# Optimization experiments

Measured on AMD Instinct MI355X. Metric: run time of the kernel, lower is better.

## Reference

```python
import jax, jax.numpy as jnp
import numpy as np

B, T, D, H = 256, 512, 128, 256


def setup_inputs() -> dict:
    key = jax.random.key(0)
    ks = jax.random.split(key, 8)
    return {
        "x": jax.random.normal(ks[0], (B, T, D), jnp.float32),
        "m": jax.random.randint(ks[1], (B, T, D), 0, 2, jnp.int32),
        "s": jax.random.uniform(ks[2], (B, T, 1), jnp.float32),
        "kernel": jax.random.normal(ks[3], (D, 3 * H), jnp.float32) * 0.05,
        "recurrent_kernel": jax.random.normal(ks[4], (H, 3 * H), jnp.float32) * 0.05,
        "masking_kernel": jax.random.normal(ks[5], (D, 3 * H), jnp.float32) * 0.05,
        "bias": jnp.zeros((3 * H,), jnp.float32),
        "input_decay_kernel": jax.random.normal(ks[6], (D,), jnp.float32) * 0.05,
        "input_decay_bias": jnp.zeros((D,), jnp.float32),
        "hidden_decay_kernel": jax.random.normal(ks[7], (D, H), jnp.float32) * 0.05,
        "hidden_decay_bias": jnp.zeros((H,), jnp.float32),
    }


def _grud_scan(x, m, s, kernel, recurrent_kernel, masking_kernel, bias,
               input_decay_kernel, input_decay_bias,
               hidden_decay_kernel, hidden_decay_bias):
    b, t, d = x.shape
    h = recurrent_kernel.shape[0]
    mf = m.astype(x.dtype)
    mb = m > 0  # boolean mask, K.switch semantics
    # mask projection is h-independent -> hoist the big GEMM out of the scan
    mproj = jnp.einsum('btd,dk->btk', mf, masking_kernel)  # [B,T,3H]
    Kz, Kr, Kh = kernel[:, :h], kernel[:, h:2 * h], kernel[:, 2 * h:]
    Rz, Rr, Rh = recurrent_kernel[:, :h], recurrent_kernel[:, h:2 * h], recurrent_kernel[:, 2 * h:]
    bz, br, bh = bias[:h], bias[h:2 * h], bias[2 * h:]

    def step(carry, inp):
        h_tm1, x_keep, s_prev = carry
        xt, mbt, st, mpt = inp  # xt [B,D], mbt [B,D] bool, st [B,1], mpt [B,3H]
        d_t = st - s_prev  # [B,D] via broadcast
        gamma_di = jnp.exp(-jax.nn.relu(d_t * input_decay_kernel + input_decay_bias))
        gamma_dh = jnp.exp(-jax.nn.relu(d_t @ hidden_decay_kernel + hidden_decay_bias))
        x_keep_t = jnp.where(mbt, xt, x_keep)
        x_t = jnp.where(mbt, xt, gamma_di * x_keep_t)
        h_d = gamma_dh * h_tm1
        mz, mr, mh = mpt[:, :h], mpt[:, h:2 * h], mpt[:, 2 * h:]
        z_t = jax.nn.sigmoid(x_t @ Kz + h_d @ Rz + mz + bz)
        r_pre = x_t @ Kr + h_d @ Rr + mr + br  # original uses pre-activation r in hh
        hh_t = jnp.tanh(x_t @ Kh + (r_pre * h_d) @ Rh + mh + bh)
        h_t = z_t * h_tm1 + (1.0 - z_t) * hh_t
        s_keep = jnp.where(mbt, jnp.broadcast_to(st, s_prev.shape), s_prev)
        return (h_t, x_keep_t, s_keep), h_t

    init = (jnp.zeros((b, h), x.dtype), jnp.zeros((b, d), x.dtype), jnp.zeros((b, d), x.dtype))
    xs = (jnp.swapaxes(x, 0, 1), jnp.swapaxes(mb, 0, 1),
          jnp.swapaxes(s, 0, 1), jnp.swapaxes(mproj, 0, 1))
    _, hs = jax.lax.scan(step, init, xs)  # hs: [T,B,H]
    return jnp.swapaxes(hs, 0, 1)  # [B,T,H]


def reference(x, m, s, kernel, recurrent_kernel, masking_kernel, bias,
              input_decay_kernel, input_decay_bias,
              hidden_decay_kernel, hidden_decay_bias):
    return _grud_scan(x, m, s, kernel, recurrent_kernel, masking_kernel, bias,
                      input_decay_kernel, input_decay_bias,
                      hidden_decay_kernel, hidden_decay_bias)
```

## Files before the change

### kernel.cpp

```cpp
#include <hip/hip_runtime.h>
#include <hip/hip_bf16.h>
#include <cstdint>


#define Bsz 256
#define Tsz 512
#define Dsz 128
#define Hsz 256
#define BT  (Bsz * Tsz)
#define N3H 768

typedef __attribute__((ext_vector_type(8))) short   short8;
typedef __attribute__((ext_vector_type(8))) __bf16  bf16x8;
typedef __attribute__((ext_vector_type(4))) float   f32x4;

__device__ __forceinline__ unsigned short f2bf(float f) {
    union { float f; unsigned u; } v; v.f = f;
    unsigned r = v.u + 0x7fffu + ((v.u >> 16) & 1u);
    return (unsigned short)(r >> 16);
}
__device__ __forceinline__ float b2f(unsigned short u) {
    union { unsigned u; float f; } v; v.u = ((unsigned)u) << 16;
    return v.f;
}
__device__ __forceinline__ bf16x8 ld_frag(const unsigned short* p) {
    short8 v = *(const short8*)p;
    return __builtin_bit_cast(bf16x8, v);
}

__global__ void k_pack(const float* __restrict__ kern, const float* __restrict__ maskk,
                       const float* __restrict__ rk,   const float* __restrict__ hdk,
                       unsigned short* __restrict__ KM_T, unsigned short* __restrict__ R_T,
                       unsigned short* __restrict__ W_T) {
    int i = blockIdx.x * 256 + threadIdx.x;
    if (i < N3H * 256) {
        int n = i >> 8, k = i & 255;
        float v = (k < 128) ? kern[k * N3H + n] : maskk[(k - 128) * N3H + n];
        KM_T[i] = f2bf(v);
        R_T[i]  = f2bf(rk[k * N3H + n]);
    } else {
        int j = i - N3H * 256;
        if (j < 256 * 128) {
            int n = j >> 7, k = j & 127;
            W_T[j] = f2bf(hdk[k * 256 + n]);
        }
    }
}

__global__ __launch_bounds__(256) void k_locf(
        const float* __restrict__ x, const int* __restrict__ m,
        const float* __restrict__ s, const float* __restrict__ wdi,
        const float* __restrict__ bdi,
        unsigned short* __restrict__ X2, unsigned short* __restrict__ Dt) {
    int gid = blockIdx.x * blockDim.x + threadIdx.x;
    int b = gid >> 7, d = gid & 127;
    float w  = wdi[d], bi = bdi[d];
    float x_keep = 0.f, s_prev = 0.f;
    const float* xb  = x + (size_t)b * Tsz * Dsz + d;
    const int*   mb_ = m + (size_t)b * Tsz * Dsz + d;
    const float* sb  = s + (size_t)b * Tsz;
    unsigned short* X2b = X2 + (size_t)b * Tsz * 256 + d;
    unsigned short* Dtb = Dt + (size_t)b * Tsz * 128 + d;
    for (int t0 = 0; t0 < Tsz; t0 += 4) {
        float xv[4], sv[4]; int mv[4];
#pragma unroll
        for (int u = 0; u < 4; u++) {
            xv[u] = xb[(size_t)(t0 + u) * Dsz];
            mv[u] = mb_[(size_t)(t0 + u) * Dsz];
            sv[u] = sb[t0 + u];
        }
#pragma unroll
        for (int u = 0; u < 4; u++) {
            int t = t0 + u;
            float dt  = sv[u] - s_prev;
            float gdi = __expf(-fmaxf(dt * w + bi, 0.f));
            bool  mbt = mv[u] > 0;
            if (mbt) x_keep = xv[u];
            float xe = mbt ? xv[u] : gdi * x_keep;
            if (mbt) s_prev = sv[u];
            X2b[(size_t)t * 256]       = f2bf(xe);
            X2b[(size_t)t * 256 + 128] = f2bf((float)mv[u]);
            Dtb[(size_t)t * 128]       = f2bf(dt);
        }
    }
}

template <int MODE, int K, int N>
__global__ __launch_bounds__(256) void k_gemm(
        const unsigned short* __restrict__ A, const unsigned short* __restrict__ Bt,
        const float* __restrict__ bias, unsigned short* __restrict__ C) {
    __shared__ unsigned short As[128][40];
    __shared__ unsigned short Bs[128][40];
    int m0 = blockIdx.x * 128, n0 = blockIdx.y * 128;
    int tid = threadIdx.x, lane = tid & 63, w = tid >> 6;
    int wm = w & 1, wn = w >> 1;
    int r15 = lane & 15, q = lane >> 4;
    int arow = tid >> 2, akg = tid & 3;
    f32x4 acc[4][4];
#pragma unroll
    for (int i = 0; i < 4; i++)
#pragma unroll
        for (int j = 0; j < 4; j++) acc[i][j] = f32x4{0.f, 0.f, 0.f, 0.f};

    for (int kk = 0; kk < K; kk += 32) {
        short8 av0 = *(const short8*)(A  + (size_t)(m0 + arow)      * K + kk + akg * 8);
        short8 av1 = *(const short8*)(A  + (size_t)(m0 + arow + 64) * K + kk + akg * 8);
        short8 bv0 = *(const short8*)(Bt + (size_t)(n0 + arow)      * K + kk + akg * 8);
        short8 bv1 = *(const short8*)(Bt + (size_t)(n0 + arow + 64) * K + kk + akg * 8);
        *(short8*)&As[arow][akg * 8]      = av0;
        *(short8*)&As[arow + 64][akg * 8] = av1;
        *(short8*)&Bs[arow][akg * 8]      = bv0;
        *(short8*)&Bs[arow + 64][akg * 8] = bv1;
        __syncthreads();
        bf16x8 af[4], bf[4];
#pragma unroll
        for (int i = 0; i < 4; i++) af[i] = ld_frag(&As[wm * 64 + i * 16 + r15][q * 8]);
#pragma unroll
        for (int j = 0; j < 4; j++) bf[j] = ld_frag(&Bs[wn * 64 + j * 16 + r15][q * 8]);
#pragma unroll
        for (int i = 0; i < 4; i++)
#pragma unroll
            for (int j = 0; j < 4; j++)
                acc[i][j] = __builtin_amdgcn_mfma_f32_16x16x32_bf16(af[i], bf[j], acc[i][j], 0, 0, 0);
        __syncthreads();
    }
#pragma unroll
    for (int i = 0; i < 4; i++)
#pragma unroll
        for (int j = 0; j < 4; j++) {
            int col = n0 + wn * 64 + j * 16 + r15;
            float bs = bias[col];
#pragma unroll
            for (int rg = 0; rg < 4; rg++) {
                int row = m0 + wm * 64 + i * 16 + q * 4 + rg;
                float v = acc[i][j][rg] + bs;
                if (MODE == 1) v = __expf(-fmaxf(v, 0.f));
                C[(size_t)row * N + col] = f2bf(v);
            }
        }
}

__global__ __launch_bounds__(512, 2) void k_scan(
        const unsigned short* __restrict__ Apre, const unsigned short* __restrict__ G,
        const unsigned short* __restrict__ R_T, float* __restrict__ out) {
    int b = blockIdx.x;
    int tid = threadIdx.x, lane = tid & 63, w = tid >> 6;
    int r15 = lane & 15, q = lane >> 4;

    __shared__ float h_lds[256];
    __shared__ float hd_f32[256];
    __shared__ float z_buf[256];
    __shared__ __align__(16) unsigned short hd_bf[256];
    __shared__ __align__(16) unsigned short u_bf[256];
    __shared__ __align__(16) unsigned short ap_l[2][768];
    __shared__ __align__(16) unsigned short g_l[2][256];

    bf16x8 fzr[4][8];
    bf16x8 fh[2][8];
#pragma unroll
    for (int nt = 0; nt < 4; nt++) {
        const unsigned short* base = R_T + (size_t)(w * 64 + nt * 16 + r15) * 256 + q * 8;
#pragma unroll
        for (int kt = 0; kt < 8; kt++) {
            fzr[nt][kt] = ld_frag(base + kt * 32);
            asm volatile("" : "+v"(fzr[nt][kt]));
        }
    }
#pragma unroll
    for (int nt = 0; nt < 2; nt++) {
        const unsigned short* base = R_T + (size_t)(512 + w * 32 + nt * 16 + r15) * 256 + q * 8;
#pragma unroll
        for (int kt = 0; kt < 8; kt++) {
            fh[nt][kt] = ld_frag(base + kt * 32);
            asm volatile("" : "+v"(fh[nt][kt]));
        }
    }

    if (tid < 256) { h_lds[tid] = 0.f; hd_f32[tid] = 0.f; hd_bf[tid] = 0; }

    const unsigned short* aprow = Apre + (size_t)b * Tsz * N3H;
    const unsigned short* grow  = G    + (size_t)b * Tsz * 256;

    if (tid < 192)      *(uint2*)&ap_l[0][tid * 4]         = *(const uint2*)(aprow + tid * 4);
    else if (tid < 384) *(uint2*)&ap_l[1][(tid-192) * 4]   = *(const uint2*)(aprow + N3H + (tid-192) * 4);
    else if (tid < 448) *(uint2*)&g_l[0][(tid-384) * 4]    = *(const uint2*)(grow + (tid-384) * 4);
    else                *(uint2*)&g_l[1][(tid-448) * 4]    = *(const uint2*)(grow + 256 + (tid-448) * 4);
    __syncthreads();

    float* outb = out + (size_t)b * Tsz * 256;
    for (int t = 0; t < Tsz; t++) {
        int buf = t & 1;
        int tp2 = (t + 2 < Tsz) ? t + 2 : Tsz - 1;
        unsigned pf;
        if (tid < 384) pf = *(const unsigned*)(aprow + (size_t)tp2 * N3H + tid * 2);
        else           pf = *(const unsigned*)(grow  + (size_t)tp2 * 256 + (tid - 384) * 2);

        f32x4 acc[4];
#pragma unroll
        for (int nt = 0; nt < 4; nt++) acc[nt] = f32x4{0.f, 0.f, 0.f, 0.f};
#pragma unroll
        for (int kt = 0; kt < 8; kt++) {
            bf16x8 afr = ld_frag(&hd_bf[kt * 32 + q * 8]);
#pragma unroll
            for (int nt = 0; nt < 4; nt++)
                acc[nt] = __builtin_amdgcn_mfma_f32_16x16x32_bf16(afr, fzr[nt][kt], acc[nt], 0, 0, 0);
        }
        {
            int c = w * 64 + q * 16 + r15;
            float pre = acc[q][0] + b2f(ap_l[buf][c]);
            if (w < 4) {
                z_buf[c] = 1.f / (1.f + __expf(-pre));
            } else {
                int uc = c - 256;
                u_bf[uc] = f2bf(pre * hd_f32[uc]);
            }
        }
        __syncthreads();

        f32x4 acch[2];
#pragma unroll
        for (int nt = 0; nt < 2; nt++) acch[nt] = f32x4{0.f, 0.f, 0.f, 0.f};
#pragma unroll
        for (int kt = 0; kt < 8; kt++) {
            bf16x8 afr = ld_frag(&u_bf[kt * 32 + q * 8]);
#pragma unroll
            for (int nt = 0; nt < 2; nt++)
                acch[nt] = __builtin_amdgcn_mfma_f32_16x16x32_bf16(afr, fh[nt][kt], acch[nt], 0, 0, 0);
        }
        if (lane < 32) {
            int ch = w * 32 + q * 16 + r15;
            float pre = acch[q][0] + b2f(ap_l[buf][512 + ch]);
            float e2 = __expf(2.f * pre);
            float hh = 1.f - 2.f / (e2 + 1.f);
            float z  = z_buf[ch];
            float hn = z * h_lds[ch] + (1.f - z) * hh;
            h_lds[ch] = hn;
            outb[(size_t)t * 256 + ch] = hn;
            float hdn = b2f(g_l[buf ^ 1][ch]) * hn;
            hd_f32[ch] = hdn;
            hd_bf[ch]  = f2bf(hdn);
        }
        __syncthreads();

        if (tid < 384) *(unsigned*)&ap_l[buf][tid * 2] = pf;
        else           *(unsigned*)&g_l[buf][(tid - 384) * 2] = pf;
    }
}

extern "C" void kernel_launch(void* const* d_in, const int* in_sizes, int n_in,
                              void* d_out, int out_size, void* d_ws, size_t ws_size,
                              hipStream_t stream) {
    const float* x    = (const float*)d_in[0];
    const int*   m    = (const int*)  d_in[1];
    const float* s    = (const float*)d_in[2];
    const float* kern = (const float*)d_in[3];
    const float* rk   = (const float*)d_in[4];
    const float* mk   = (const float*)d_in[5];
    const float* bias = (const float*)d_in[6];
    const float* wdi  = (const float*)d_in[7];
    const float* bdi  = (const float*)d_in[8];
    const float* hdk  = (const float*)d_in[9];
    const float* hdb  = (const float*)d_in[10];
    float* out = (float*)d_out;

    char* ws = (char*)d_ws;
    size_t off = 0;
    auto alloc = [&](size_t bytes) -> void* {
        void* p = ws + off; off += (bytes + 255) & ~(size_t)255; return p;
    };
    unsigned short* X2   = (unsigned short*)alloc((size_t)BT * 256 * 2);
    unsigned short* Dt   = (unsigned short*)alloc((size_t)BT * 128 * 2);
    unsigned short* Apre = (unsigned short*)alloc((size_t)BT * N3H * 2);
    unsigned short* Gm   = (unsigned short*)alloc((size_t)BT * 256 * 2);
    unsigned short* KM_T = (unsigned short*)alloc((size_t)N3H * 256 * 2);
    unsigned short* R_T  = (unsigned short*)alloc((size_t)N3H * 256 * 2);
    unsigned short* W_T  = (unsigned short*)alloc((size_t)256 * 128 * 2);
    (void)ws_size; (void)in_sizes; (void)n_in; (void)out_size;

    k_pack<<<dim3((N3H * 256 + 256 * 128 + 255) / 256), dim3(256), 0, stream>>>(
        kern, mk, rk, hdk, KM_T, R_T, W_T);
    k_locf<<<dim3(Bsz * Dsz / 256), dim3(256), 0, stream>>>(x, m, s, wdi, bdi, X2, Dt);
    k_gemm<0, 256, N3H><<<dim3(BT / 128, N3H / 128), dim3(256), 0, stream>>>(X2, KM_T, bias, Apre);
    k_gemm<1, 128, 256><<<dim3(BT / 128, 256 / 128), dim3(256), 0, stream>>>(Dt, W_T, hdb, Gm);
    k_scan<<<dim3(Bsz), dim3(512), 0, stream>>>(Apre, Gm, R_T, out);
}
```

Before: 1.116 ms.

## Deepen scan prefetch, use raw barriers, pin weights in AGPRs, direct-to-LDS GEMM loads

The scan kernel moves to a 4-slot LDS ring with a prefetch distance of three steps. Each global load gets an extra iteration before its value is stored to LDS, so that latency is hidden. Its __syncthreads calls become a raw s_barrier that waits only on lgkmcnt, which avoids waiting on outstanding global loads. The recurrent weight fragments are pinned in AGPRs, and the LDS reads of gate inputs are hoisted ahead of the MFMA chains. The GEMM uses global_load_lds to load tiles straight into unpadded LDS, which may add bank conflicts when fragments are read.

```diff
diff --git a/kernel.cpp b/kernel.cpp
--- a/kernel.cpp
+++ b/kernel.cpp
@@ -26,6 +26,9 @@
 __device__ __forceinline__ bf16x8 ld_frag(const unsigned short* p) {
     short8 v = *(const short8*)p;
     return __builtin_bit_cast(bf16x8, v);
+}
+__device__ __forceinline__ void rawbar() {
+    asm volatile("s_waitcnt lgkmcnt(0)\n\ts_barrier" ::: "memory");
 }
 
 __global__ void k_pack(const float* __restrict__ kern, const float* __restrict__ maskk,
@@ -89,13 +92,12 @@
 __global__ __launch_bounds__(256) void k_gemm(
         const unsigned short* __restrict__ A, const unsigned short* __restrict__ Bt,
         const float* __restrict__ bias, unsigned short* __restrict__ C) {
-    __shared__ unsigned short As[128][40];
-    __shared__ unsigned short Bs[128][40];
+    __shared__ __align__(16) unsigned short As[128 * 32];
+    __shared__ __align__(16) unsigned short Bs[128 * 32];
     int m0 = blockIdx.x * 128, n0 = blockIdx.y * 128;
     int tid = threadIdx.x, lane = tid & 63, w = tid >> 6;
     int wm = w & 1, wn = w >> 1;
     int r15 = lane & 15, q = lane >> 4;
-    int arow = tid >> 2, akg = tid & 3;
     f32x4 acc[4][4];
 #pragma unroll
     for (int i = 0; i < 4; i++)
@@ -103,20 +105,25 @@
         for (int j = 0; j < 4; j++) acc[i][j] = f32x4{0.f, 0.f, 0.f, 0.f};
 
     for (int kk = 0; kk < K; kk += 32) {
-        short8 av0 = *(const short8*)(A  + (size_t)(m0 + arow)      * K + kk + akg * 8);
-        short8 av1 = *(const short8*)(A  + (size_t)(m0 + arow + 64) * K + kk + akg * 8);
-        short8 bv0 = *(const short8*)(Bt + (size_t)(n0 + arow)      * K + kk + akg * 8);
-        short8 bv1 = *(const short8*)(Bt + (size_t)(n0 + arow + 64) * K + kk + akg * 8);
-        *(short8*)&As[arow][akg * 8]      = av0;
-        *(short8*)&As[arow + 64][akg * 8] = av1;
-        *(short8*)&Bs[arow][akg * 8]      = bv0;
-        *(short8*)&Bs[arow + 64][akg * 8] = bv1;
+#pragma unroll
+        for (int j = 0; j < 2; j++) {
+            int chunk = (w * 2 + j) * 64 + lane;
+            int row = chunk >> 2, ko = (chunk & 3) * 8;
+            __builtin_amdgcn_global_load_lds(
+                (const __attribute__((address_space(1))) void*)(A + (size_t)(m0 + row) * K + kk + ko),
+                (__attribute__((address_space(3))) void*)(As + (size_t)(w * 2 + j) * 512),
+                16, 0, 0);
+            __builtin_amdgcn_global_load_lds(
+                (const __attribute__((address_space(1))) void*)(Bt + (size_t)(n0 + row) * K + kk + ko),
+                (__attribute__((address_space(3))) void*)(Bs + (size_t)(w * 2 + j) * 512),
+                16, 0, 0);
+        }
         __syncthreads();
         bf16x8 af[4], bf[4];
 #pragma unroll
-        for (int i = 0; i < 4; i++) af[i] = ld_frag(&As[wm * 64 + i * 16 + r15][q * 8]);
-#pragma unroll
-        for (int j = 0; j < 4; j++) bf[j] = ld_frag(&Bs[wn * 64 + j * 16 + r15][q * 8]);
+        for (int i = 0; i < 4; i++) af[i] = ld_frag(&As[(wm * 64 + i * 16 + r15) * 32 + q * 8]);
+#pragma unroll
+        for (int j = 0; j < 4; j++) bf[j] = ld_frag(&Bs[(wn * 64 + j * 16 + r15) * 32 + q * 8]);
 #pragma unroll
         for (int i = 0; i < 4; i++)
 #pragma unroll
@@ -152,8 +159,8 @@
     __shared__ float z_buf[256];
     __shared__ __align__(16) unsigned short hd_bf[256];
     __shared__ __align__(16) unsigned short u_bf[256];
-    __shared__ __align__(16) unsigned short ap_l[2][768];
-    __shared__ __align__(16) unsigned short g_l[2][256];
+    __shared__ __align__(16) unsigned short ap_l[4][768];
+    __shared__ __align__(16) unsigned short g_l[4][256];
 
     bf16x8 fzr[4][8];
     bf16x8 fh[2][8];
@@ -163,7 +170,7 @@
 #pragma unroll
         for (int kt = 0; kt < 8; kt++) {
             fzr[nt][kt] = ld_frag(base + kt * 32);
-            asm volatile("" : "+v"(fzr[nt][kt]));
+            asm volatile("" : "+a"(fzr[nt][kt]));
         }
     }
 #pragma unroll
@@ -172,7 +179,7 @@
 #pragma unroll
         for (int kt = 0; kt < 8; kt++) {
             fh[nt][kt] = ld_frag(base + kt * 32);
-            asm volatile("" : "+v"(fh[nt][kt]));
+            asm volatile("" : "+a"(fh[nt][kt]));
         }
     }
 
@@ -181,19 +188,31 @@
     const unsigned short* aprow = Apre + (size_t)b * Tsz * N3H;
     const unsigned short* grow  = G    + (size_t)b * Tsz * 256;
 
-    if (tid < 192)      *(uint2*)&ap_l[0][tid * 4]         = *(const uint2*)(aprow + tid * 4);
-    else if (tid < 384) *(uint2*)&ap_l[1][(tid-192) * 4]   = *(const uint2*)(aprow + N3H + (tid-192) * 4);
-    else if (tid < 448) *(uint2*)&g_l[0][(tid-384) * 4]    = *(const uint2*)(grow + (tid-384) * 4);
-    else                *(uint2*)&g_l[1][(tid-448) * 4]    = *(const uint2*)(grow + 256 + (tid-448) * 4);
+    if (tid < 384) {
+        *(unsigned*)&ap_l[0][tid * 2] = *(const unsigned*)(aprow + tid * 2);
+        *(unsigned*)&ap_l[1][tid * 2] = *(const unsigned*)(aprow + N3H + tid * 2);
+    } else {
+        int t2 = tid - 384;
+        *(unsigned*)&g_l[0][t2 * 2] = *(const unsigned*)(grow + t2 * 2);
+        *(unsigned*)&g_l[1][t2 * 2] = *(const unsigned*)(grow + 256 + t2 * 2);
+    }
+    unsigned pf_old;
+    if (tid < 384) pf_old = *(const unsigned*)(aprow + (size_t)2 * N3H + tid * 2);
+    else           pf_old = *(const unsigned*)(grow + (size_t)2 * 256 + (tid - 384) * 2);
     __syncthreads();
 
     float* outb = out + (size_t)b * Tsz * 256;
+    int c2 = w * 64 + q * 16 + r15;
+    int ch = w * 32 + (q & 1) * 16 + r15;
     for (int t = 0; t < Tsz; t++) {
-        int buf = t & 1;
-        int tp2 = (t + 2 < Tsz) ? t + 2 : Tsz - 1;
-        unsigned pf;
-        if (tid < 384) pf = *(const unsigned*)(aprow + (size_t)tp2 * N3H + tid * 2);
-        else           pf = *(const unsigned*)(grow  + (size_t)tp2 * 256 + (tid - 384) * 2);
+        int buf = t & 3;
+        int tp3 = (t + 3 < Tsz) ? t + 3 : Tsz - 1;
+        unsigned pf_new;
+        if (tid < 384) pf_new = *(const unsigned*)(aprow + (size_t)tp3 * N3H + tid * 2);
+        else           pf_new = *(const unsigned*)(grow  + (size_t)tp3 * 256 + (tid - 384) * 2);
+
+        float apz = b2f(ap_l[buf][c2]);
+        float hdp = hd_f32[c2 & 255];
 
         f32x4 acc[4];
 #pragma unroll
@@ -206,17 +225,16 @@
                 acc[nt] = __builtin_amdgcn_mfma_f32_16x16x32_bf16(afr, fzr[nt][kt], acc[nt], 0, 0, 0);
         }
         {
-            int c = w * 64 + q * 16 + r15;
-            float pre = acc[q][0] + b2f(ap_l[buf][c]);
-            if (w < 4) {
-                z_buf[c] = 1.f / (1.f + __expf(-pre));
-            } else {
-                int uc = c - 256;
-                u_bf[uc] = f2bf(pre * hd_f32[uc]);
-            }
-        }
-        __syncthreads();
-
+            float pre = acc[q][0] + apz;
+            if (w < 4) z_buf[c2] = 1.f / (1.f + __expf(-pre));
+            else       u_bf[c2 - 256] = f2bf(pre * hdp);
+        }
+        rawbar();
+
+        float aph   = b2f(ap_l[buf][512 + ch]);
+        float hprev = h_lds[ch];
+        float gnext = b2f(g_l[(t + 1) & 3][ch]);
+        float zv    = z_buf[ch];
         f32x4 acch[2];
 #pragma unroll
         for (int nt = 0; nt < 2; nt++) acch[nt] = f32x4{0.f, 0.f, 0.f, 0.f};
@@ -228,22 +246,21 @@
                 acch[nt] = __builtin_amdgcn_mfma_f32_16x16x32_bf16(afr, fh[nt][kt], acch[nt], 0, 0, 0);
         }
         if (lane < 32) {
-            int ch = w * 32 + q * 16 + r15;
-            float pre = acch[q][0] + b2f(ap_l[buf][512 + ch]);
+            float pre = acch[q][0] + aph;
             float e2 = __expf(2.f * pre);
             float hh = 1.f - 2.f / (e2 + 1.f);
-            float z  = z_buf[ch];
-            float hn = z * h_lds[ch] + (1.f - z) * hh;
+            float hn = zv * hprev + (1.f - zv) * hh;
             h_lds[ch] = hn;
             outb[(size_t)t * 256 + ch] = hn;
-            float hdn = b2f(g_l[buf ^ 1][ch]) * hn;
+            float hdn = gnext * hn;
             hd_f32[ch] = hdn;
             hd_bf[ch]  = f2bf(hdn);
         }
-        __syncthreads();
-
-        if (tid < 384) *(unsigned*)&ap_l[buf][tid * 2] = pf;
-        else           *(unsigned*)&g_l[buf][(tid - 384) * 2] = pf;
+        rawbar();
+
+        if (tid < 384) *(unsigned*)&ap_l[(t + 2) & 3][tid * 2] = pf_old;
+        else           *(unsigned*)&g_l[(t + 2) & 3][(tid - 384) * 2] = pf_old;
+        pf_old = pf_new;
     }
 }
 
```

Result: slower. 1.151 ms (+3.2%).
